# Kernel optimization log

Measured on AMD Instinct MI355X. Metric: run time of the kernel, lower is better.

The kernel has to match this reference:

```python
import jax, jax.numpy as jnp
import numpy as np

D_EMB_IN = 1024
D_K = 64
D_EMB_OUT = 1024
NB_HEADS = 16


def setup_inputs() -> dict:
    key = jax.random.key(0)
    k1, k2, k3, k4, k5 = jax.random.split(key, 5)
    scale = 0.02
    X = jax.random.normal(k1, (2, 2048, D_EMB_IN), dtype=jnp.float32)
    # nn.Linear weights are [out, in]; we store them transposed-ready as [in, out]
    Wq = jax.random.normal(k2, (D_EMB_IN, NB_HEADS * D_K), dtype=jnp.float32) * scale
    Wk = jax.random.normal(k3, (D_EMB_IN, NB_HEADS * D_K), dtype=jnp.float32) * scale
    Wv = jax.random.normal(k4, (D_EMB_IN, NB_HEADS * D_K), dtype=jnp.float32) * scale
    Wo = jax.random.normal(k5, (NB_HEADS * D_K, D_EMB_OUT), dtype=jnp.float32) * scale
    return {"X": X, "Wq": Wq, "Wk": Wk, "Wv": Wv, "Wo": Wo}


def reference(X, Wq, Wk, Wv, Wo):
    B, T, _ = X.shape
    H, Dk = NB_HEADS, D_K
    # project and split heads: [B, H, T, Dk]
    def proj(W):
        return (X @ W).reshape(B, T, H, Dk).transpose(0, 2, 1, 3)
    Q, K, V = proj(Wq), proj(Wk), proj(Wv)
    S = jnp.einsum("bhqd,bhkd->bhqk", Q, K) / jnp.sqrt(jnp.float32(Dk))
    causal = jnp.tril(jnp.ones((T, T), dtype=bool))  # True = keep
    S = jnp.where(causal, S, -jnp.inf)
    P = jax.nn.softmax(S, axis=-1)
    A = jnp.einsum("bhqk,bhkd->bhqd", P, V)
    A = A.transpose(0, 2, 1, 3).reshape(B, T, H * Dk)
    return A @ Wo
```

## Files before the change

kernel.cpp:

```cpp
#include <hip/hip_runtime.h>
#include <hip/hip_bf16.h>


typedef unsigned short u16;
typedef __bf16 bf16x8 __attribute__((ext_vector_type(8)));
typedef float f32x4 __attribute__((ext_vector_type(4)));
typedef u16 u16x4 __attribute__((ext_vector_type(4)));

#define TS 72
#define PS 136
#define NEG_INF (-1e30f)
#define SC_LOG2 0.1803368801f

#if __has_builtin(__builtin_amdgcn_exp2f)
#define EXP2(x) __builtin_amdgcn_exp2f(x)
#else
#define EXP2(x) exp2f(x)
#endif

#define GLD_LDS16(gp, lp) __builtin_amdgcn_global_load_lds( \
    (const __attribute__((address_space(1))) void*)(gp),    \
    (__attribute__((address_space(3))) void*)(lp), 16, 0, 0)

__device__ __forceinline__ bf16x8 as_bf16x8(int4 v) { return __builtin_bit_cast(bf16x8, v); }
__device__ __forceinline__ u16 bf16_bits(float f) { return __builtin_bit_cast(u16, (__bf16)f); }

__device__ __forceinline__ bool detect_f32(const void* X) {
    const u16* x16 = (const u16*)X;
    int lane = threadIdx.x & 63;
    int hits = 0;
#pragma unroll
    for (int i = 0; i < 4; ++i) {
        u16 v = x16[lane * 4 + i];
        hits += (((v >> 7) & 0xFF) > 130) ? 1 : 0;
    }
    return __popcll(__ballot(hits > 0)) >= 8;
}

__device__ __forceinline__ bf16x8 load8(const void* p, size_t eoff, bool f32m) {
    if (!f32m) return as_bf16x8(*(const int4*)((const u16*)p + eoff));
    const float* f = (const float*)p + eoff;
    float4 a = *(const float4*)f;
    float4 b = *(const float4*)(f + 4);
    bf16x8 r;
    r[0] = (__bf16)a.x; r[1] = (__bf16)a.y; r[2] = (__bf16)a.z; r[3] = (__bf16)a.w;
    r[4] = (__bf16)b.x; r[5] = (__bf16)b.y; r[6] = (__bf16)b.z; r[7] = (__bf16)b.w;
    return r;
}

__global__ __launch_bounds__(256) void prep_all(const void* __restrict__ Wq,
                                                const void* __restrict__ Wk,
                                                const void* __restrict__ Wv,
                                                const void* __restrict__ Wo,
                                                const void* __restrict__ X,
                                                u16* __restrict__ Wt3,
                                                u16* __restrict__ Wot,
                                                u16* __restrict__ Xbf) {
    bool f32m = detect_f32(X);
    int z = blockIdx.z;
    if (z == 4) {
        int blk = blockIdx.y * 16 + blockIdx.x;
        size_t base = (size_t)blk * 16384 + threadIdx.x * 8;
#pragma unroll
        for (int i = 0; i < 8; ++i) {
            size_t eoff = base + (size_t)i * 2048;
            bf16x8 v = load8(X, eoff, f32m);
            *(int4*)(Xbf + eoff) = __builtin_bit_cast(int4, v);
        }
        return;
    }
    const void* in = (z == 0) ? Wq : (z == 1) ? Wk : (z == 2) ? Wv : Wo;
    u16* out = (z < 3) ? (Wt3 + (size_t)z * (1u << 20)) : Wot;
    __shared__ alignas(16) u16 T[64][TS];
    int r0 = blockIdx.y * 64, c0 = blockIdx.x * 64;
    int tr = threadIdx.x >> 3, tc8 = threadIdx.x & 7;
    bf16x8 v0 = load8(in, (size_t)(r0 + tr) * 1024 + c0 + tc8 * 8, f32m);
    bf16x8 v1 = load8(in, (size_t)(r0 + tr + 32) * 1024 + c0 + tc8 * 8, f32m);
    *(int4*)&T[tr][tc8 * 8]      = __builtin_bit_cast(int4, v0);
    *(int4*)&T[tr + 32][tc8 * 8] = __builtin_bit_cast(int4, v1);
    __syncthreads();
    for (int half = 0; half < 2; ++half) {
        int cr = tr + half * 32;
        u16 tmp[8];
#pragma unroll
        for (int i = 0; i < 8; ++i) tmp[i] = T[tc8 * 8 + i][cr];
        *(int4*)(out + (size_t)(c0 + cr) * 1024 + r0 + tc8 * 8) = *(int4*)tmp;
    }
}

__global__ __launch_bounds__(256, 4) void gemm128(const u16* __restrict__ A,
                                                  const u16* __restrict__ Bt,
                                                  u16* __restrict__ Cq, u16* __restrict__ Ck,
                                                  u16* __restrict__ Cv) {
    __shared__ alignas(16) u16 As[128 * 64];
    __shared__ alignas(16) u16 Bs[128 * 64];
    const int K = 1024;
    int tid = threadIdx.x, wave = tid >> 6, lane = tid & 63;
    int quad = lane >> 4, l16 = lane & 15;
    int wrow = wave >> 1, wcol = wave & 1;
    int m0 = blockIdx.x * 128, n0 = blockIdx.y * 128;
    int rlane = lane >> 3, kc = lane & 7;
    int scol = (kc ^ rlane) * 8;

    f32x4 acc[4][4] = {};

    for (int k0 = 0; k0 < K; k0 += 64) {
        __syncthreads();
#pragma unroll
        for (int i = 0; i < 4; ++i) {
            int rc = wave * 4 + i;
            GLD_LDS16(A  + (size_t)(m0 + rc * 8 + rlane) * K + k0 + scol, As + rc * 512);
            GLD_LDS16(Bt + (size_t)(n0 + rc * 8 + rlane) * K + k0 + scol, Bs + rc * 512);
        }
        __syncthreads();
#pragma unroll
        for (int ks = 0; ks < 2; ++ks) {
            bf16x8 af[4], bfr[4];
#pragma unroll
            for (int i = 0; i < 4; ++i) {
                int row = wrow * 64 + i * 16 + l16;
                af[i] = as_bf16x8(*(const int4*)(As + row * 64 + (((ks * 4 + quad) ^ (row & 7)) * 8)));
            }
#pragma unroll
            for (int j = 0; j < 4; ++j) {
                int row = wcol * 64 + j * 16 + l16;
                bfr[j] = as_bf16x8(*(const int4*)(Bs + row * 64 + (((ks * 4 + quad) ^ (row & 7)) * 8)));
            }
#pragma unroll
            for (int i = 0; i < 4; ++i)
#pragma unroll
                for (int j = 0; j < 4; ++j)
                    acc[i][j] = __builtin_amdgcn_mfma_f32_16x16x32_bf16(af[i], bfr[j], acc[i][j], 0, 0, 0);
        }
    }

#pragma unroll
    for (int i = 0; i < 4; ++i)
#pragma unroll
        for (int j = 0; j < 4; ++j)
#pragma unroll
            for (int r = 0; r < 4; ++r) {
                int m = m0 + wrow * 64 + i * 16 + quad * 4 + r;
                int n = n0 + wcol * 64 + j * 16 + l16;
                float f = acc[i][j][r];
                if (n < 1024)       Cq[(size_t)m * 1024 + n] = bf16_bits(f);
                else if (n < 2048)  Ck[(size_t)m * 1024 + n - 1024] = bf16_bits(f);
                else {
                    int n2 = n - 2048;
                    int bh = ((m >> 11) << 4) | (n2 >> 6), d = n2 & 63, t = m & 2047;
                    Cv[(((size_t)bh * 64 + d) << 11) + t] = bf16_bits(f);
                }
            }
}

__global__ __launch_bounds__(256, 4) void gemm_out(const u16* __restrict__ A,
                                                   const u16* __restrict__ Bt,
                                                   void* __restrict__ Cout,
                                                   const void* __restrict__ Xdet) {
    bool f32m = detect_f32(Xdet);
    __shared__ alignas(16) u16 As[64 * 128];
    __shared__ alignas(16) u16 Bs[128 * 128];
    const int K = 1024;
    int tid = threadIdx.x, wave = tid >> 6, lane = tid & 63;
    int quad = lane >> 4, l16 = lane & 15;
    int wrow = wave & 1, wcol = wave >> 1;
    int m0 = blockIdx.x * 64, n0 = blockIdx.y * 128;
    int rlane4 = lane >> 4, kc16 = lane & 15;

    f32x4 acc[2][4] = {};

    for (int k0 = 0; k0 < K; k0 += 128) {
        __syncthreads();
#pragma unroll
        for (int i = 0; i < 8; ++i) {
            int rb = wave * 32 + i * 4;
            int grow = rb + rlane4;
            int gch = kc16 ^ (grow & 15);
            GLD_LDS16(Bt + (size_t)(n0 + grow) * K + k0 + gch * 8, Bs + rb * 128);
        }
#pragma unroll
        for (int i = 0; i < 4; ++i) {
            int rb = wave * 16 + i * 4;
            int grow = rb + rlane4;
            int gch = kc16 ^ (grow & 15);
            GLD_LDS16(A + (size_t)(m0 + grow) * K + k0 + gch * 8, As + rb * 128);
        }
        __syncthreads();
#pragma unroll
        for (int ks = 0; ks < 4; ++ks) {
            bf16x8 af[2], bfr[4];
#pragma unroll
            for (int i = 0; i < 2; ++i) {
                int row = wrow * 32 + i * 16 + l16;
                af[i] = as_bf16x8(*(const int4*)(As + row * 128 + (((ks * 4 + quad) ^ (row & 15)) * 8)));
            }
#pragma unroll
            for (int j = 0; j < 4; ++j) {
                int row = wcol * 64 + j * 16 + l16;
                bfr[j] = as_bf16x8(*(const int4*)(Bs + row * 128 + (((ks * 4 + quad) ^ (row & 15)) * 8)));
            }
#pragma unroll
            for (int i = 0; i < 2; ++i)
#pragma unroll
                for (int j = 0; j < 4; ++j)
                    acc[i][j] = __builtin_amdgcn_mfma_f32_16x16x32_bf16(af[i], bfr[j], acc[i][j], 0, 0, 0);
        }
    }

#pragma unroll
    for (int i = 0; i < 2; ++i)
#pragma unroll
        for (int j = 0; j < 4; ++j)
#pragma unroll
            for (int r = 0; r < 4; ++r) {
                int m = m0 + wrow * 32 + i * 16 + quad * 4 + r;
                int n = n0 + wcol * 64 + j * 16 + l16;
                float f = acc[i][j][r];
                if (f32m) ((float*)Cout)[(size_t)m * 1024 + n] = f;
                else      ((u16*)Cout)[(size_t)m * 1024 + n] = bf16_bits(f);
            }
}

__global__ __launch_bounds__(512, 4) void attn_kernel(const u16* __restrict__ Qb,
                                                      const u16* __restrict__ Kb,
                                                      const u16* __restrict__ Vt,
                                                      u16* __restrict__ Ab) {
    __shared__ alignas(16) u16 Ks[128 * 64];
    __shared__ alignas(16) u16 Vs[64 * 128];
    __shared__ alignas(16) u16 Ps[128 * PS];

    int tid = threadIdx.x, wave = tid >> 6, lane = tid & 63;
    int quad = lane >> 4, l16 = lane & 15;
    int bh = blockIdx.x;
    int J = (blockIdx.y < 8) ? (15 - (int)blockIdx.y) : ((int)blockIdx.y - 8);
    int b = bh >> 4, h = bh & 15;
    int q0 = J * 128;
    int kr4 = lane >> 3, kc = lane & 7;
    int vr4 = lane >> 4, vc = lane & 15;

    const u16* qrow = Qb + (size_t)(b * 2048 + q0 + wave * 16 + l16) * 1024 + h * 64;
    bf16x8 qa0 = as_bf16x8(*(const int4*)(qrow + quad * 8));
    bf16x8 qa1 = as_bf16x8(*(const int4*)(qrow + 32 + quad * 8));

    f32x4 o[4] = {};
    float psum = 0.0f;

    const u16* kbase = Kb + (size_t)(b * 2048) * 1024 + h * 64;
    const u16* vbase = Vt + (size_t)bh * 64 * 2048;

    for (int j2 = 0; j2 <= J; ++j2) {
        int t0 = j2 * 128;
        __syncthreads();
#pragma unroll
        for (int i = 0; i < 2; ++i) {
            int rb = (wave * 2 + i) * 8;
            int grow = rb + kr4;
            int gch = kc ^ (grow & 7);
            GLD_LDS16(kbase + (size_t)(t0 + grow) * 1024 + gch * 8, Ks + rb * 64);
        }
#pragma unroll
        for (int i = 0; i < 2; ++i) {
            int rb = (wave * 2 + i) * 4;
            int grow = rb + vr4;
            int gch = vc ^ (grow & 15);
            GLD_LDS16(vbase + (size_t)grow * 2048 + t0 + gch * 8, Vs + rb * 128);
        }
        __syncthreads();

        bool diag = (j2 == J);
        int ntc = diag ? ((wave & ~1) + 2) : 8;

        f32x4 s[8];
        __builtin_amdgcn_s_setprio(1);
#pragma unroll
        for (int nt = 0; nt < 8; ++nt) {
            if (nt >= ntc) continue;
            if (diag && nt > wave) {
                s[nt][0] = NEG_INF; s[nt][1] = NEG_INF; s[nt][2] = NEG_INF; s[nt][3] = NEG_INF;
                continue;
            }
            int row = nt * 16 + l16;
            int sw = row & 7;
            f32x4 a = {};
            bf16x8 b0 = as_bf16x8(*(const int4*)(Ks + row * 64 + ((quad ^ sw) * 8)));
            a = __builtin_amdgcn_mfma_f32_16x16x32_bf16(b0, qa0, a, 0, 0, 0);
            bf16x8 b1 = as_bf16x8(*(const int4*)(Ks + row * 64 + (((4 + quad) ^ sw) * 8)));
            a = __builtin_amdgcn_mfma_f32_16x16x32_bf16(b1, qa1, a, 0, 0, 0);
            a = a * SC_LOG2;
            if (diag && nt == wave) {
#pragma unroll
                for (int r = 0; r < 4; ++r)
                    if (quad * 4 + r > l16) a[r] = NEG_INF;
            }
            s[nt] = a;
        }
        __builtin_amdgcn_s_setprio(0);

        int prow = (wave * 16 + l16) * PS;
#pragma unroll
        for (int nt = 0; nt < 8; ++nt) {
            if (nt >= ntc) continue;
            u16x4 pk;
            float ps4 = 0.0f;
#pragma unroll
            for (int r = 0; r < 4; ++r) {
                float p = EXP2(s[nt][r]);
                ps4 += p;
                pk[r] = bf16_bits(p);
            }
            psum += ps4;
            *(u16x4*)(Ps + prow + nt * 16 + quad * 4) = pk;
        }

        int ksm = ntc >> 1;
        __builtin_amdgcn_s_setprio(1);
#pragma unroll
        for (int ks = 0; ks < 4; ++ks) {
            if (ks >= ksm) continue;
            bf16x8 pa = as_bf16x8(*(const int4*)(Ps + (wave * 16 + l16) * PS + ks * 32 + quad * 8));
#pragma unroll
            for (int d4 = 0; d4 < 4; ++d4) {
                int vrow = d4 * 16 + l16;
                bf16x8 vb = as_bf16x8(*(const int4*)(Vs + vrow * 128 + (((ks * 4 + quad) ^ l16) * 8)));
                o[d4] = __builtin_amdgcn_mfma_f32_16x16x32_bf16(pa, vb, o[d4], 0, 0, 0);
            }
        }
        __builtin_amdgcn_s_setprio(0);
    }

    psum += __shfl_xor(psum, 16);
    psum += __shfl_xor(psum, 32);

    u16* arow = Ab + (size_t)(b * 2048 + q0 + wave * 16) * 1024 + h * 64;
#pragma unroll
    for (int r = 0; r < 4; ++r) {
        float dn = __shfl(psum, quad * 4 + r, 16);
        float inv = 1.0f / dn;
#pragma unroll
        for (int d4 = 0; d4 < 4; ++d4)
            arow[(quad * 4 + r) * 1024 + d4 * 16 + l16] = bf16_bits(o[d4][r] * inv);
    }
}

extern "C" void kernel_launch(void* const* d_in, const int* in_sizes, int n_in,
                              void* d_out, int out_size, void* d_ws, size_t ws_size,
                              hipStream_t stream) {
    (void)in_sizes; (void)n_in; (void)out_size; (void)ws_size;
    const void* X  = d_in[0];
    const void* Wq = d_in[1];
    const void* Wk = d_in[2];
    const void* Wv = d_in[3];
    const void* Wo = d_in[4];
    u16* ws16 = (u16*)d_ws;
    const size_t M1 = 1u << 20;
    u16* Xbf = ws16 + 0 * M1;
    u16* Wt3 = ws16 + 4 * M1;
    u16* Qb  = ws16 + 7 * M1;
    u16* Kb  = ws16 + 11 * M1;
    u16* Vt  = ws16 + 15 * M1;
    u16* Wot = ws16 + 19 * M1;
    u16* Ab  = ws16 + 0 * M1;

    prep_all<<<dim3(16, 16, 5), 256, 0, stream>>>(Wq, Wk, Wv, Wo, X, Wt3, Wot, Xbf);
    gemm128<<<dim3(32, 24), 256, 0, stream>>>(Xbf, Wt3, Qb, Kb, Vt);
    attn_kernel<<<dim3(32, 16), 512, 0, stream>>>(Qb, Kb, Vt, Ab);
    gemm_out<<<dim3(64, 8), 256, 0, stream>>>(Ab, Wot, d_out, X);
}
```

Before: 168.3 us.

## Use 256-key tiles and interleave QK, softmax and PV per 32-key group

Doubles the K/V tile staged in LDS per iteration from 128 to 256 keys, which halves the number of loop trips and block-wide barriers. Score computation, exp2 and the PV MFMA now run per 32-key group, so only a small per-wave P scratch (56-element stride) is needed instead of a full 128x136 buffer. The extra K/V shared memory is roughly offset by the smaller P buffer. For even J the last tile loads 128 keys beyond the causal range that are never used, which adds wasted load traffic. The finer-grained interleaving may also reduce overlap between MFMA and exp work inside each wave.

```diff
diff --git a/kernel.cpp b/kernel.cpp
--- a/kernel.cpp
+++ b/kernel.cpp
@@ -8,7 +8,7 @@
 typedef u16 u16x4 __attribute__((ext_vector_type(4)));
 
 #define TS 72
-#define PS 136
+#define PSQ 56
 #define NEG_INF (-1e30f)
 #define SC_LOG2 0.1803368801f
 
@@ -225,9 +225,9 @@
                                                       const u16* __restrict__ Kb,
                                                       const u16* __restrict__ Vt,
                                                       u16* __restrict__ Ab) {
-    __shared__ alignas(16) u16 Ks[128 * 64];
-    __shared__ alignas(16) u16 Vs[64 * 128];
-    __shared__ alignas(16) u16 Ps[128 * PS];
+    __shared__ alignas(16) u16 Ks[256 * 64];
+    __shared__ alignas(16) u16 Vs[64 * 256];
+    __shared__ alignas(16) u16 Ps[128 * PSQ];
 
     int tid = threadIdx.x, wave = tid >> 6, lane = tid & 63;
     int quad = lane >> 4, l16 = lane & 15;
@@ -236,7 +236,7 @@
     int b = bh >> 4, h = bh & 15;
     int q0 = J * 128;
     int kr4 = lane >> 3, kc = lane & 7;
-    int vr4 = lane >> 4, vc = lane & 15;
+    int vr2 = lane >> 5, vc32 = lane & 31;
 
     const u16* qrow = Qb + (size_t)(b * 2048 + q0 + wave * 16 + l16) * 1024 + h * 64;
     bf16x8 qa0 = as_bf16x8(*(const int4*)(qrow + quad * 8));
@@ -244,88 +244,92 @@
 
     f32x4 o[4] = {};
     float psum = 0.0f;
+    int prow = (wave * 16 + l16) * PSQ;
 
     const u16* kbase = Kb + (size_t)(b * 2048) * 1024 + h * 64;
     const u16* vbase = Vt + (size_t)bh * 64 * 2048;
 
-    for (int j2 = 0; j2 <= J; ++j2) {
-        int t0 = j2 * 128;
-        __syncthreads();
-#pragma unroll
-        for (int i = 0; i < 2; ++i) {
-            int rb = (wave * 2 + i) * 8;
+    int NJ = (J + 2) >> 1;
+
+    for (int j2 = 0; j2 < NJ; ++j2) {
+        int t0 = j2 * 256;
+        __syncthreads();
+#pragma unroll
+        for (int i = 0; i < 4; ++i) {
+            int rb = wave * 32 + i * 8;
             int grow = rb + kr4;
             int gch = kc ^ (grow & 7);
             GLD_LDS16(kbase + (size_t)(t0 + grow) * 1024 + gch * 8, Ks + rb * 64);
         }
 #pragma unroll
-        for (int i = 0; i < 2; ++i) {
-            int rb = (wave * 2 + i) * 4;
-            int grow = rb + vr4;
-            int gch = vc ^ (grow & 15);
-            GLD_LDS16(vbase + (size_t)grow * 2048 + t0 + gch * 8, Vs + rb * 128);
-        }
-        __syncthreads();
-
-        bool diag = (j2 == J);
-        int ntc = diag ? ((wave & ~1) + 2) : 8;
-
-        f32x4 s[8];
-        __builtin_amdgcn_s_setprio(1);
-#pragma unroll
-        for (int nt = 0; nt < 8; ++nt) {
-            if (nt >= ntc) continue;
-            if (diag && nt > wave) {
-                s[nt][0] = NEG_INF; s[nt][1] = NEG_INF; s[nt][2] = NEG_INF; s[nt][3] = NEG_INF;
-                continue;
-            }
-            int row = nt * 16 + l16;
-            int sw = row & 7;
-            f32x4 a = {};
-            bf16x8 b0 = as_bf16x8(*(const int4*)(Ks + row * 64 + ((quad ^ sw) * 8)));
-            a = __builtin_amdgcn_mfma_f32_16x16x32_bf16(b0, qa0, a, 0, 0, 0);
-            bf16x8 b1 = as_bf16x8(*(const int4*)(Ks + row * 64 + (((4 + quad) ^ sw) * 8)));
-            a = __builtin_amdgcn_mfma_f32_16x16x32_bf16(b1, qa1, a, 0, 0, 0);
-            a = a * SC_LOG2;
-            if (diag && nt == wave) {
-#pragma unroll
-                for (int r = 0; r < 4; ++r)
-                    if (quad * 4 + r > l16) a[r] = NEG_INF;
-            }
-            s[nt] = a;
-        }
-        __builtin_amdgcn_s_setprio(0);
-
-        int prow = (wave * 16 + l16) * PS;
-#pragma unroll
-        for (int nt = 0; nt < 8; ++nt) {
-            if (nt >= ntc) continue;
-            u16x4 pk;
-            float ps4 = 0.0f;
-#pragma unroll
-            for (int r = 0; r < 4; ++r) {
-                float p = EXP2(s[nt][r]);
-                ps4 += p;
-                pk[r] = bf16_bits(p);
-            }
-            psum += ps4;
-            *(u16x4*)(Ps + prow + nt * 16 + quad * 4) = pk;
-        }
-
-        int ksm = ntc >> 1;
-        __builtin_amdgcn_s_setprio(1);
-#pragma unroll
-        for (int ks = 0; ks < 4; ++ks) {
-            if (ks >= ksm) continue;
-            bf16x8 pa = as_bf16x8(*(const int4*)(Ps + (wave * 16 + l16) * PS + ks * 32 + quad * 8));
-#pragma unroll
-            for (int d4 = 0; d4 < 4; ++d4) {
-                int vrow = d4 * 16 + l16;
-                bf16x8 vb = as_bf16x8(*(const int4*)(Vs + vrow * 128 + (((ks * 4 + quad) ^ l16) * 8)));
-                o[d4] = __builtin_amdgcn_mfma_f32_16x16x32_bf16(pa, vb, o[d4], 0, 0, 0);
-            }
-        }
-        __builtin_amdgcn_s_setprio(0);
+        for (int i = 0; i < 4; ++i) {
+            int rb = wave * 8 + i * 2;
+            int grow = rb + vr2;
+            int gch = vc32 ^ (grow & 15);
+            GLD_LDS16(vbase + (size_t)grow * 2048 + t0 + gch * 8, Vs + rb * 256);
+        }
+        __syncthreads();
+
+        int lim = 8 * J + wave - 16 * j2;
+        int ntc = (lim + 2) & ~1;
+        if (ntc > 16) ntc = 16;
+
+#pragma unroll
+        for (int g = 0; g < 8; ++g) {
+            if (2 * g >= ntc) continue;
+            f32x4 sg0, sg1;
+            __builtin_amdgcn_s_setprio(1);
+#pragma unroll
+            for (int h2 = 0; h2 < 2; ++h2) {
+                int nt = 2 * g + h2;
+                f32x4 a = {};
+                if (nt > lim) {
+                    a[0] = NEG_INF; a[1] = NEG_INF; a[2] = NEG_INF; a[3] = NEG_INF;
+                } else {
+                    int row = nt * 16 + l16;
+                    int sw = row & 7;
+                    bf16x8 b0 = as_bf16x8(*(const int4*)(Ks + row * 64 + ((quad ^ sw) * 8)));
+                    a = __builtin_amdgcn_mfma_f32_16x16x32_bf16(b0, qa0, a, 0, 0, 0);
+                    bf16x8 b1 = as_bf16x8(*(const int4*)(Ks + row * 64 + (((4 + quad) ^ sw) * 8)));
+                    a = __builtin_amdgcn_mfma_f32_16x16x32_bf16(b1, qa1, a, 0, 0, 0);
+                    a = a * SC_LOG2;
+                    if (nt == lim) {
+#pragma unroll
+                        for (int r = 0; r < 4; ++r)
+                            if (quad * 4 + r > l16) a[r] = NEG_INF;
+                    }
+                }
+                if (h2 == 0) sg0 = a; else sg1 = a;
+            }
+            __builtin_amdgcn_s_setprio(0);
+
+#pragma unroll
+            for (int h2 = 0; h2 < 2; ++h2) {
+                f32x4 sv = h2 ? sg1 : sg0;
+                u16x4 pk;
+                float ps4 = 0.0f;
+#pragma unroll
+                for (int r = 0; r < 4; ++r) {
+                    float p = EXP2(sv[r]);
+                    ps4 += p;
+                    pk[r] = bf16_bits(p);
+                }
+                psum += ps4;
+                *(u16x4*)(Ps + prow + h2 * 16 + quad * 4) = pk;
+            }
+
+            __builtin_amdgcn_s_setprio(1);
+            {
+                bf16x8 pa = as_bf16x8(*(const int4*)(Ps + prow + quad * 8));
+#pragma unroll
+                for (int d4 = 0; d4 < 4; ++d4) {
+                    int vrow = d4 * 16 + l16;
+                    bf16x8 vb = as_bf16x8(*(const int4*)(Vs + vrow * 256 + (((g * 4 + quad) ^ l16) * 8)));
+                    o[d4] = __builtin_amdgcn_mfma_f32_16x16x32_bf16(pa, vb, o[d4], 0, 0, 0);
+                }
+            }
+            __builtin_amdgcn_s_setprio(0);
+        }
     }
 
     psum += __shfl_xor(psum, 16);
```

Result: no change. 168.4 us (+0.0%).
